# Optimization experiments

Hardware: AMD Instinct MI355X
Metric: run time of the kernel (lower is better)

Reference implementation:

```python
import jax, jax.numpy as jnp
import numpy as np

DIM = 1024
HEADS = 8
DIM_HEAD = 64
EPS = 1e-10
LN_EPS = 1e-5


def setup_inputs() -> dict:
    key = jax.random.key(0)
    k1, k2, k3 = jax.random.split(key, 3)
    b, n = 2, 4096
    x = jax.random.normal(k1, (b, n, DIM), dtype=jnp.float32)
    ln_gamma = jnp.ones((DIM,), dtype=jnp.float32)
    ln_beta = jnp.zeros((DIM,), dtype=jnp.float32)
    w_qkv = jax.random.normal(k2, (DIM, 3 * HEADS * DIM_HEAD), dtype=jnp.float32) * (DIM ** -0.5)
    w_out = jax.random.normal(k3, (HEADS * DIM_HEAD, DIM), dtype=jnp.float32) * ((HEADS * DIM_HEAD) ** -0.5)
    return {"x": x, "ln_gamma": ln_gamma, "ln_beta": ln_beta, "w_qkv": w_qkv, "w_out": w_out}


def _layernorm(x, gamma, beta):
    mu = jnp.mean(x, axis=-1, keepdims=True)
    var = jnp.var(x, axis=-1, keepdims=True)
    return (x - mu) * jax.lax.rsqrt(var + LN_EPS) * gamma + beta


def reference(x, ln_gamma, ln_beta, w_qkv, w_out):
    b, n, _ = x.shape
    h, dh = HEADS, DIM_HEAD
    scale = dh ** -0.5

    xn = _layernorm(x, ln_gamma, ln_beta)          # prenorm
    qkv = xn @ w_qkv                               # [b, n, 3*h*dh]
    q, k, v = jnp.split(qkv, 3, axis=-1)
    # [b, n, h*dh] -> [b, h, n, dh]
    def to_heads(t):
        return t.reshape(b, n, h, dh).transpose(0, 2, 1, 3)
    q, k, v = to_heads(q), to_heads(k), to_heads(v)

    # Ring/blockwise attention with online softmax is mathematically
    # equivalent to full softmax attention with an eps in the denominator.
    sim = jnp.einsum('bhid,bhjd->bhij', q, k) * scale   # [b, h, n, n]
    causal_mask = jnp.tril(jnp.ones((n, n), dtype=bool))
    sim = jnp.where(causal_mask, sim, -jnp.finfo(sim.dtype).max)

    m = jnp.max(sim, axis=-1, keepdims=True)            # row max (stable)
    p = jnp.exp(sim - m)
    denom = jnp.sum(p, axis=-1, keepdims=True) + EPS
    attn = p / denom

    out = jnp.einsum('bhij,bhjd->bhid', attn, v)        # [b, h, n, dh]
    out = out.transpose(0, 2, 1, 3).reshape(b, n, h * dh)
    return out @ w_out                                  # [b, n, dim]
```

## Files before the change

kernel.cpp:

```cpp
#include <hip/hip_runtime.h>
#include <hip/hip_bf16.h>
#include <stdint.h>

typedef unsigned short u16;
typedef unsigned int u32;

typedef __attribute__((ext_vector_type(8))) __bf16 bf16x8;
typedef __attribute__((ext_vector_type(4))) float f32x4;
typedef __attribute__((ext_vector_type(8))) u16 u16x8;

#define DIM 1024
#define SEQ 4096
#define NTOK 8192
#define NBH 16
#define NSLOT 136

static __device__ __forceinline__ float bf2f(u16 u) {
    union { u32 u; float f; } c; c.u = ((u32)u) << 16; return c.f;
}
static __device__ __forceinline__ u16 f2bf(float f) {
    union { float f; u32 u; } c; c.f = f;
    u32 u = c.u;
    return (u16)((u + 0x7FFF + ((u >> 16) & 1)) >> 16);
}
static __device__ __forceinline__ u16 cvt_bf16(float f) {
    union { __bf16 b; u16 u; } c; c.b = (__bf16)f;
    return c.u;
}
static __device__ __forceinline__ u32 pack_bf16(float lo, float hi) {
    return (u32)cvt_bf16(lo) | ((u32)cvt_bf16(hi) << 16);
}
static __device__ __forceinline__ f32x4 mfma_bf16(bf16x8 a, bf16x8 b, f32x4 c) {
    return __builtin_amdgcn_mfma_f32_16x16x32_bf16(a, b, c, 0, 0, 0);
}

typedef const __attribute__((address_space(1))) unsigned int* gptr_t;
typedef __attribute__((address_space(3))) unsigned int* lptr_t;

__global__ __launch_bounds__(256) void ln_kernel(const float* __restrict__ x,
                                                 const float* __restrict__ g,
                                                 const float* __restrict__ bta,
                                                 u16* __restrict__ xn) {
    int row = blockIdx.x;
    int tid = threadIdx.x;
    float4 v = ((const float4*)(x + (size_t)row * DIM))[tid];
    float f[4] = {v.x, v.y, v.z, v.w};
    float s = 0.f, s2 = 0.f;
#pragma unroll
    for (int i = 0; i < 4; i++) { s += f[i]; s2 += f[i] * f[i]; }
#pragma unroll
    for (int m = 1; m < 64; m <<= 1) { s += __shfl_xor(s, m); s2 += __shfl_xor(s2, m); }
    __shared__ float red[8];
    int w = tid >> 6;
    if ((tid & 63) == 0) { red[w * 2] = s; red[w * 2 + 1] = s2; }
    __syncthreads();
    s  = red[0] + red[2] + red[4] + red[6];
    s2 = red[1] + red[3] + red[5] + red[7];
    float mu = s * (1.f / DIM);
    float var = s2 * (1.f / DIM) - mu * mu;
    float rstd = rsqrtf(var + 1e-5f);
    u16 o[4];
#pragma unroll
    for (int i = 0; i < 4; i++) {
        int c = tid * 4 + i;
        o[i] = f2bf((f[i] - mu) * rstd * g[c] + bta[c]);
    }
    *(uint64_t*)(xn + (size_t)row * DIM + tid * 4) = *(uint64_t*)o;
}

__global__ __launch_bounds__(256) void transpose_kernel(const float* __restrict__ src,
                                                        u16* __restrict__ dst,
                                                        int R, int C) {
    __shared__ float t[32][33];
    int lx = threadIdx.x & 31, ly = threadIdx.x >> 5;
    int c = blockIdx.x * 32 + lx;
#pragma unroll
    for (int i = 0; i < 32; i += 8)
        t[ly + i][lx] = src[(size_t)(blockIdx.y * 32 + ly + i) * C + c];
    __syncthreads();
    int rr = blockIdx.y * 32 + lx;
#pragma unroll
    for (int i = 0; i < 32; i += 8)
        dst[(size_t)(blockIdx.x * 32 + ly + i) * R + rr] = f2bf(t[lx][ly + i]);
}

template <int K>
static __device__ __forceinline__ void gemm_core(const u16* __restrict__ A,
                                                 const u16* __restrict__ B,
                                                 int rowBase, int colBase,
                                                 u16* A_lds, u16* B_lds,
                                                 f32x4 acc[4][4]) {
    int tid = threadIdx.x;
    int lane = tid & 63;
    int l15 = lane & 15, q4 = lane >> 4;
    int w = tid >> 6;
    int wm = w >> 1, wn = w & 1;
#pragma unroll
    for (int mt = 0; mt < 4; mt++)
#pragma unroll
        for (int nt = 0; nt < 4; nt++) acc[mt][nt] = (f32x4){0.f, 0.f, 0.f, 0.f};

    char* Ab = (char*)A_lds;
    char* Bb = (char*)B_lds;

    for (int k0 = 0; k0 < K; k0 += 32) {
        __syncthreads();
#pragma unroll
        for (int i = 0; i < 2; i++) {
            int c = i * 256 + tid;
            int r = c >> 2;
            int piece = (c & 3) * 8;
            const u16* gA = A + (size_t)(rowBase + r) * K + k0 + piece;
            const u16* gB = B + (size_t)(colBase + r) * K + k0 + piece;
            unsigned ldsOff = (unsigned)(i * 4096 + w * 1024);
            __builtin_amdgcn_global_load_lds((gptr_t)gA, (lptr_t)(Ab + ldsOff), 16, 0, 0);
            __builtin_amdgcn_global_load_lds((gptr_t)gB, (lptr_t)(Bb + ldsOff), 16, 0, 0);
        }
        __syncthreads();
        bf16x8 a[4], b[4];
#pragma unroll
        for (int mt = 0; mt < 4; mt++)
            a[mt] = *(const bf16x8*)(A_lds + (wm * 64 + mt * 16 + l15) * 32 + q4 * 8);
#pragma unroll
        for (int nt = 0; nt < 4; nt++)
            b[nt] = *(const bf16x8*)(B_lds + (wn * 64 + nt * 16 + l15) * 32 + q4 * 8);
#pragma unroll
        for (int mt = 0; mt < 4; mt++)
#pragma unroll
            for (int nt = 0; nt < 4; nt++)
                acc[mt][nt] = mfma_bf16(a[mt], b[nt], acc[mt][nt]);
    }
}

__global__ __launch_bounds__(256) void gemm_qkv_kernel(const u16* __restrict__ xn,
                                                       const u16* __restrict__ wT,
                                                       u16* __restrict__ qb,
                                                       u16* __restrict__ kb,
                                                       u16* __restrict__ vbT) {
    __shared__ u16 A_lds[128 * 32];
    __shared__ u16 B_lds[128 * 32];
    f32x4 acc[4][4];
    gemm_core<1024>(xn, wT, blockIdx.x * 128, blockIdx.y * 128, A_lds, B_lds, acc);
    int lane = threadIdx.x & 63;
    int w = threadIdx.x >> 6;
    int wm = w >> 1, wn = w & 1;
    const float SC = 0.125f * 1.44269504f;
#pragma unroll
    for (int mt = 0; mt < 4; mt++) {
#pragma unroll
        for (int nt = 0; nt < 4; nt++) {
#pragma unroll
            for (int r = 0; r < 4; r++) {
                int m = blockIdx.x * 128 + wm * 64 + mt * 16 + (lane >> 4) * 4 + r;
                int n = blockIdx.y * 128 + wn * 64 + nt * 16 + (lane & 15);
                int piece = n >> 9;
                int c = n & 511;
                int h = c >> 6;
                int d = c & 63;
                int bi = m >> 12;
                int nn = m & 4095;
                int bh = bi * 8 + h;
                float av = acc[mt][nt][r];
                if (piece == 0)      qb[((size_t)(bh * SEQ + nn) << 6) + d] = f2bf(av * SC);
                else if (piece == 1) kb[((size_t)(bh * SEQ + nn) << 6) + d] = f2bf(av);
                else                 vbT[((size_t)(bh * 64 + d) << 12) + nn] = f2bf(av);
            }
        }
    }
}

__global__ __launch_bounds__(256) void gemm_out_kernel(const u16* __restrict__ aout,
                                                       const u16* __restrict__ wT,
                                                       float* __restrict__ out) {
    __shared__ u16 A_lds[128 * 32];
    __shared__ u16 B_lds[128 * 32];
    f32x4 acc[4][4];
    gemm_core<512>(aout, wT, blockIdx.x * 128, blockIdx.y * 128, A_lds, B_lds, acc);
    int lane = threadIdx.x & 63;
    int w = threadIdx.x >> 6;
    int wm = w >> 1, wn = w & 1;
#pragma unroll
    for (int mt = 0; mt < 4; mt++) {
#pragma unroll
        for (int nt = 0; nt < 4; nt++) {
#pragma unroll
            for (int r = 0; r < 4; r++) {
                int m = blockIdx.x * 128 + wm * 64 + mt * 16 + (lane >> 4) * 4 + r;
                int n = blockIdx.y * 128 + wn * 64 + nt * 16 + (lane & 15);
                out[(size_t)m * DIM + n] = acc[mt][nt][r];
            }
        }
    }
}


__global__ __launch_bounds__(256) void attn_partial_kernel(const u16* __restrict__ qb,
                                                           const u16* __restrict__ kb,
                                                           const u16* __restrict__ vbT,
                                                           u16* __restrict__ part,
                                                           float* __restrict__ lpart) {
    __shared__ u16 K_lds[4096];
    __shared__ u16 V_lds[4096];
    __shared__ u16 P_lds[4][1024];

    int bid = blockIdx.x;
    int bs = (bid & 7) * 272 + (bid >> 3);
    int idx = NBH * NSLOT - 1 - bs;
    int bh = idx / NSLOT;
    int s  = idx - bh * NSLOT;
    int qt, ci;
    if (s < 20)       { qt = s; ci = 0; }
    else if (s < 60)  { int t = s - 20;  qt = 20 + (t >> 1); ci = t & 1; }
    else if (s < 120) { int t = s - 60;  qt = 40 + t / 3;    ci = t - (t / 3) * 3; }
    else              { int t = s - 120; qt = 60 + (t >> 2); ci = t & 3; }
    int nq = qt + 1;
    int nc = (nq + 19) / 20;
    int L  = nq / nc;
    int R  = nq - L * nc;
    int kt0 = ci * L + (ci < R ? ci : R);
    int kt1 = kt0 + L + (ci < R ? 1 : 0) - 1;

    int tid = threadIdx.x;
    int lane = tid & 63;
    int l15 = lane & 15, g = lane >> 4;
    int w = tid >> 6;
    int swz = (l15 & 7) << 3;
    int rd0 = (g * 8) ^ swz;
    int rd1 = (32 + g * 8) ^ swz;

    const u16* Kp0 = kb + (size_t)bh * SEQ * 64;
    const u16* VTp = vbT + (size_t)bh * 64 * SEQ;

    const u16* qp = qb + ((size_t)bh * SEQ + (size_t)qt * 64 + w * 16 + l15) * 64;
    bf16x8 bQ0 = *(const bf16x8*)(qp + g * 8);
    bf16x8 bQ1 = *(const bf16x8*)(qp + 32 + g * 8);

    int c0 = tid, c1 = tid + 256;
    int r0 = c0 >> 3, g0 = c0 & 7;
    int r1 = c1 >> 3, g1 = c1 & 7;
    int wc0 = r0 * 64 + ((g0 ^ (r0 & 7)) * 8);
    int wc1 = r1 * 64 + ((g1 ^ (r1 & 7)) * 8);

    u16x8 krA0, krA1, vrA0, vrA1;
    {
        const u16* Kt = Kp0 + (size_t)kt0 * 4096;
        krA0 = *(const u16x8*)(Kt + r0 * 64 + g0 * 8);
        krA1 = *(const u16x8*)(Kt + r1 * 64 + g1 * 8);
        vrA0 = *(const u16x8*)(VTp + (size_t)r0 * SEQ + kt0 * 64 + g0 * 8);
        vrA1 = *(const u16x8*)(VTp + (size_t)r1 * SEQ + kt0 * 64 + g1 * 8);
    }

    f32x4 Oacc[4];
    f32x4 l_acc = (f32x4){0.f, 0.f, 0.f, 0.f};
#pragma unroll
    for (int vt = 0; vt < 4; vt++) Oacc[vt] = (f32x4){0.f, 0.f, 0.f, 0.f};

    const __bf16 one_bf = (__bf16)1.0f;
    bf16x8 vones = {one_bf, one_bf, one_bf, one_bf, one_bf, one_bf, one_bf, one_bf};

    u16* Pw = &P_lds[w][0];

    for (int kt = kt0; kt <= kt1; kt++) {
        __syncthreads();
        *(u16x8*)(K_lds + wc0) = krA0;
        *(u16x8*)(K_lds + wc1) = krA1;
        *(u16x8*)(V_lds + wc0) = vrA0;
        *(u16x8*)(V_lds + wc1) = vrA1;
        __syncthreads();
        int ktn = (kt < kt1) ? kt + 1 : kt1;
        {
            const u16* Ktn = Kp0 + (size_t)ktn * 4096;
            krA0 = *(const u16x8*)(Ktn + r0 * 64 + g0 * 8);
            krA1 = *(const u16x8*)(Ktn + r1 * 64 + g1 * 8);
            vrA0 = *(const u16x8*)(VTp + (size_t)r0 * SEQ + ktn * 64 + g0 * 8);
            vrA1 = *(const u16x8*)(VTp + (size_t)r1 * SEQ + ktn * 64 + g1 * 8);
        }

        f32x4 sv[4];
#pragma unroll
        for (int nt = 0; nt < 4; nt++) {
            int row = nt * 16 + l15;
            bf16x8 a0 = *(const bf16x8*)(K_lds + row * 64 + rd0);
            bf16x8 a1 = *(const bf16x8*)(K_lds + row * 64 + rd1);
            f32x4 z = (f32x4){0.f, 0.f, 0.f, 0.f};
            z = mfma_bf16(a0, bQ0, z);
            z = mfma_bf16(a1, bQ1, z);
            sv[nt] = z;
        }

        if (kt != qt) {
#pragma unroll
            for (int nt = 0; nt < 4; nt++) {
                uint2 t;
                t.x = pack_bf16(__builtin_amdgcn_exp2f(sv[nt][0]),
                                __builtin_amdgcn_exp2f(sv[nt][1]));
                t.y = pack_bf16(__builtin_amdgcn_exp2f(sv[nt][2]),
                                __builtin_amdgcn_exp2f(sv[nt][3]));
                *(uint2*)(Pw + l15 * 64 + ((nt * 16 + g * 4) ^ swz)) = t;
            }
        } else {
            int qg = w * 16 + l15;
#pragma unroll
            for (int nt = 0; nt < 4; nt++) {
                float p[4];
#pragma unroll
                for (int r = 0; r < 4; r++) {
                    int kg = nt * 16 + g * 4 + r;
                    p[r] = (kg <= qg) ? __builtin_amdgcn_exp2f(sv[nt][r]) : 0.f;
                }
                uint2 t;
                t.x = pack_bf16(p[0], p[1]);
                t.y = pack_bf16(p[2], p[3]);
                *(uint2*)(Pw + l15 * 64 + ((nt * 16 + g * 4) ^ swz)) = t;
            }
        }

        bf16x8 aP0 = *(const bf16x8*)(Pw + l15 * 64 + rd0);
        bf16x8 aP1 = *(const bf16x8*)(Pw + l15 * 64 + rd1);
        l_acc = mfma_bf16(aP0, vones, l_acc);
        l_acc = mfma_bf16(aP1, vones, l_acc);
#pragma unroll
        for (int vt = 0; vt < 4; vt++) {
            int vrow = vt * 16 + l15;
            bf16x8 bV0 = *(const bf16x8*)(V_lds + vrow * 64 + rd0);
            bf16x8 bV1 = *(const bf16x8*)(V_lds + vrow * 64 + rd1);
            Oacc[vt] = mfma_bf16(aP0, bV0, Oacc[vt]);
            Oacc[vt] = mfma_bf16(aP1, bV1, Oacc[vt]);
        }
    }

    u16* po = part + (size_t)idx * 4096;
#pragma unroll
    for (int vt = 0; vt < 4; vt++)
#pragma unroll
        for (int r = 0; r < 4; r++) {
            int q = w * 16 + g * 4 + r;
            int d = vt * 16 + l15;
            po[q * 64 + d] = f2bf(Oacc[vt][r]);
        }
    if (l15 == 0) {
#pragma unroll
        for (int r = 0; r < 4; r++)
            lpart[(size_t)idx * 64 + w * 16 + g * 4 + r] = l_acc[r];
    }
}

__global__ __launch_bounds__(256) void attn_combine_kernel(const u16* __restrict__ part,
                                                           const float* __restrict__ lpart,
                                                           u16* __restrict__ aout) {
    int bid = blockIdx.x;
    int bh = bid >> 6;
    int qt = bid & 63;
    int nc, base;
    if (qt < 20)      { nc = 1; base = qt; }
    else if (qt < 40) { nc = 2; base = 20 + (qt - 20) * 2; }
    else if (qt < 60) { nc = 3; base = 60 + (qt - 40) * 3; }
    else              { nc = 4; base = 120 + (qt - 60) * 4; }
    int sb = bh * NSLOT + base;

    int t = threadIdx.x;
    int q = t >> 2;
    int dg = (t & 3) * 16;

    float acc[16];
#pragma unroll
    for (int j = 0; j < 16; j++) acc[j] = 0.f;
    float ll = 0.f;
    for (int ci = 0; ci < nc; ci++) {
        const u16* pp = part + (size_t)(sb + ci) * 4096 + q * 64 + dg;
        u16x8 v0 = *(const u16x8*)pp;
        u16x8 v1 = *(const u16x8*)(pp + 8);
#pragma unroll
        for (int j = 0; j < 8; j++) { acc[j] += bf2f(v0[j]); acc[8 + j] += bf2f(v1[j]); }
        ll += lpart[(size_t)(sb + ci) * 64 + q];
    }
    float inv = 1.f / (ll + 1e-10f);
    int b = bh >> 3, h = bh & 7;
    size_t row = (size_t)(b * SEQ + qt * 64 + q);
    u16 o[16];
#pragma unroll
    for (int j = 0; j < 16; j++) o[j] = f2bf(acc[j] * inv);
    u16* dst = aout + row * 512 + h * 64 + dg;
    *(u16x8*)dst = *(u16x8*)o;
    *(u16x8*)(dst + 8) = *(u16x8*)(o + 8);
}

extern "C" void kernel_launch(void* const* d_in, const int* in_sizes, int n_in,
                              void* d_out, int out_size, void* d_ws, size_t ws_size,
                              hipStream_t stream) {
    const float* x    = (const float*)d_in[0];
    const float* g    = (const float*)d_in[1];
    const float* bta  = (const float*)d_in[2];
    const float* wqkv = (const float*)d_in[3];
    const float* wout = (const float*)d_in[4];
    float* out = (float*)d_out;

    char* ws = (char*)d_ws;
    size_t off = 0;
    auto alloc = [&](size_t bytes) {
        void* p = ws + off;
        off += (bytes + 255) & ~(size_t)255;
        return p;
    };
    u16* xn    = (u16*)alloc((size_t)NTOK * DIM * 2);
    u16* wqkvT = (u16*)alloc((size_t)1536 * 1024 * 2);
    u16* woutT = (u16*)alloc((size_t)1024 * 512 * 2);
    u16* qb    = (u16*)alloc((size_t)NBH * SEQ * 64 * 2);
    u16* kb    = (u16*)alloc((size_t)NBH * SEQ * 64 * 2);
    u16* vbT   = (u16*)alloc((size_t)NBH * SEQ * 64 * 2);
    u16* part  = xn;
    float* lpart = (float*)(xn + (size_t)NBH * NSLOT * 4096);
    u16* aout  = qb;

    ln_kernel<<<NTOK, 256, 0, stream>>>(x, g, bta, xn);
    transpose_kernel<<<dim3(1536 / 32, 1024 / 32), 256, 0, stream>>>(wqkv, wqkvT, 1024, 1536);
    transpose_kernel<<<dim3(1024 / 32, 512 / 32), 256, 0, stream>>>(wout, woutT, 512, 1024);
    gemm_qkv_kernel<<<dim3(64, 12), 256, 0, stream>>>(xn, wqkvT, qb, kb, vbT);
    attn_partial_kernel<<<NBH * NSLOT, 256, 0, stream>>>(qb, kb, vbT, part, lpart);
    attn_combine_kernel<<<NBH * 64, 256, 0, stream>>>(part, lpart, aout);
    gemm_out_kernel<<<dim3(64, 8), 256, 0, stream>>>(aout, woutT, out);
}
```

Baseline: 216.1 us.

## Halve attention block to two waves with two query subtiles each; merge prep kernels

The attention partial kernel now runs with 128 threads, and each wave handles 32 query rows as two 16-row subtiles. K fragments read from LDS are reused across both subtiles, and the V fragments are reused across both output accumulators, which cuts LDS reads per MFMA. Each thread loads twice as many K/V chunks per tile, and register pressure rises. LayerNorm and the two weight transposes are also merged into one launch to save launch overhead.

```diff
diff --git a/kernel.cpp b/kernel.cpp
--- a/kernel.cpp
+++ b/kernel.cpp
@@ -37,51 +37,60 @@
 typedef const __attribute__((address_space(1))) unsigned int* gptr_t;
 typedef __attribute__((address_space(3))) unsigned int* lptr_t;
 
-__global__ __launch_bounds__(256) void ln_kernel(const float* __restrict__ x,
-                                                 const float* __restrict__ g,
-                                                 const float* __restrict__ bta,
-                                                 u16* __restrict__ xn) {
-    int row = blockIdx.x;
+__global__ __launch_bounds__(256) void prep_kernel(const float* __restrict__ x,
+                                                   const float* __restrict__ g,
+                                                   const float* __restrict__ bta,
+                                                   u16* __restrict__ xn,
+                                                   const float* __restrict__ wqkv,
+                                                   u16* __restrict__ wqkvT,
+                                                   const float* __restrict__ wout,
+                                                   u16* __restrict__ woutT) {
+    __shared__ float red[8];
+    __shared__ float tT[32][33];
+    int bid = blockIdx.x;
     int tid = threadIdx.x;
-    float4 v = ((const float4*)(x + (size_t)row * DIM))[tid];
-    float f[4] = {v.x, v.y, v.z, v.w};
-    float s = 0.f, s2 = 0.f;
-#pragma unroll
-    for (int i = 0; i < 4; i++) { s += f[i]; s2 += f[i] * f[i]; }
-#pragma unroll
-    for (int m = 1; m < 64; m <<= 1) { s += __shfl_xor(s, m); s2 += __shfl_xor(s2, m); }
-    __shared__ float red[8];
-    int w = tid >> 6;
-    if ((tid & 63) == 0) { red[w * 2] = s; red[w * 2 + 1] = s2; }
+
+    if (bid < NTOK) {
+        int row = bid;
+        float4 v = ((const float4*)(x + (size_t)row * DIM))[tid];
+        float f[4] = {v.x, v.y, v.z, v.w};
+        float s = 0.f, s2 = 0.f;
+#pragma unroll
+        for (int i = 0; i < 4; i++) { s += f[i]; s2 += f[i] * f[i]; }
+#pragma unroll
+        for (int m = 1; m < 64; m <<= 1) { s += __shfl_xor(s, m); s2 += __shfl_xor(s2, m); }
+        int w = tid >> 6;
+        if ((tid & 63) == 0) { red[w * 2] = s; red[w * 2 + 1] = s2; }
+        __syncthreads();
+        s  = red[0] + red[2] + red[4] + red[6];
+        s2 = red[1] + red[3] + red[5] + red[7];
+        float mu = s * (1.f / DIM);
+        float var = s2 * (1.f / DIM) - mu * mu;
+        float rstd = rsqrtf(var + 1e-5f);
+        u16 o[4];
+#pragma unroll
+        for (int i = 0; i < 4; i++) {
+            int c = tid * 4 + i;
+            o[i] = f2bf((f[i] - mu) * rstd * g[c] + bta[c]);
+        }
+        *(uint64_t*)(xn + (size_t)row * DIM + tid * 4) = *(uint64_t*)o;
+        return;
+    }
+
+    int tt = bid - NTOK;
+    const float* src; u16* dst; int R, C, bx, by;
+    if (tt < 1536) { src = wqkv; dst = wqkvT; R = 1024; C = 1536; bx = tt % 48; by = tt / 48; }
+    else { tt -= 1536; src = wout; dst = woutT; R = 512; C = 1024; bx = tt & 31; by = tt >> 5; }
+    int lx = tid & 31, ly = tid >> 5;
+    int c = bx * 32 + lx;
+#pragma unroll
+    for (int i = 0; i < 32; i += 8)
+        tT[ly + i][lx] = src[(size_t)(by * 32 + ly + i) * C + c];
     __syncthreads();
-    s  = red[0] + red[2] + red[4] + red[6];
-    s2 = red[1] + red[3] + red[5] + red[7];
-    float mu = s * (1.f / DIM);
-    float var = s2 * (1.f / DIM) - mu * mu;
-    float rstd = rsqrtf(var + 1e-5f);
-    u16 o[4];
-#pragma unroll
-    for (int i = 0; i < 4; i++) {
-        int c = tid * 4 + i;
-        o[i] = f2bf((f[i] - mu) * rstd * g[c] + bta[c]);
-    }
-    *(uint64_t*)(xn + (size_t)row * DIM + tid * 4) = *(uint64_t*)o;
-}
-
-__global__ __launch_bounds__(256) void transpose_kernel(const float* __restrict__ src,
-                                                        u16* __restrict__ dst,
-                                                        int R, int C) {
-    __shared__ float t[32][33];
-    int lx = threadIdx.x & 31, ly = threadIdx.x >> 5;
-    int c = blockIdx.x * 32 + lx;
+    int rr = by * 32 + lx;
 #pragma unroll
     for (int i = 0; i < 32; i += 8)
-        t[ly + i][lx] = src[(size_t)(blockIdx.y * 32 + ly + i) * C + c];
-    __syncthreads();
-    int rr = blockIdx.y * 32 + lx;
-#pragma unroll
-    for (int i = 0; i < 32; i += 8)
-        dst[(size_t)(blockIdx.x * 32 + ly + i) * R + rr] = f2bf(t[lx][ly + i]);
+        dst[(size_t)(bx * 32 + ly + i) * R + rr] = f2bf(tT[lx][ly + i]);
 }
 
 template <int K>
@@ -194,14 +203,14 @@
 }
 
 
-__global__ __launch_bounds__(256) void attn_partial_kernel(const u16* __restrict__ qb,
+__global__ __launch_bounds__(128) void attn_partial_kernel(const u16* __restrict__ qb,
                                                            const u16* __restrict__ kb,
                                                            const u16* __restrict__ vbT,
                                                            u16* __restrict__ part,
                                                            float* __restrict__ lpart) {
     __shared__ u16 K_lds[4096];
     __shared__ u16 V_lds[4096];
-    __shared__ u16 P_lds[4][1024];
+    __shared__ u16 P_lds[2][1024];
 
     int bid = blockIdx.x;
     int bs = (bid & 7) * 272 + (bid >> 3);
@@ -231,29 +240,43 @@
     const u16* Kp0 = kb + (size_t)bh * SEQ * 64;
     const u16* VTp = vbT + (size_t)bh * 64 * SEQ;
 
-    const u16* qp = qb + ((size_t)bh * SEQ + (size_t)qt * 64 + w * 16 + l15) * 64;
-    bf16x8 bQ0 = *(const bf16x8*)(qp + g * 8);
-    bf16x8 bQ1 = *(const bf16x8*)(qp + 32 + g * 8);
-
-    int c0 = tid, c1 = tid + 256;
-    int r0 = c0 >> 3, g0 = c0 & 7;
-    int r1 = c1 >> 3, g1 = c1 & 7;
-    int wc0 = r0 * 64 + ((g0 ^ (r0 & 7)) * 8);
-    int wc1 = r1 * 64 + ((g1 ^ (r1 & 7)) * 8);
-
-    u16x8 krA0, krA1, vrA0, vrA1;
+    bf16x8 bQ[2][2];
+#pragma unroll
+    for (int qs = 0; qs < 2; qs++) {
+        const u16* qp = qb + ((size_t)bh * SEQ + (size_t)qt * 64 + w * 32 + qs * 16 + l15) * 64;
+        bQ[qs][0] = *(const bf16x8*)(qp + g * 8);
+        bQ[qs][1] = *(const bf16x8*)(qp + 32 + g * 8);
+    }
+
+    int wcc[4], soK[4];
+    size_t soV[4];
+#pragma unroll
+    for (int i = 0; i < 4; i++) {
+        int c = tid + 128 * i;
+        int r = c >> 3, gg = c & 7;
+        wcc[i] = r * 64 + ((gg ^ (r & 7)) * 8);
+        soK[i] = r * 64 + gg * 8;
+        soV[i] = (size_t)r * SEQ + gg * 8;
+    }
+
+    u16x8 krA[4], vrA[4];
     {
         const u16* Kt = Kp0 + (size_t)kt0 * 4096;
-        krA0 = *(const u16x8*)(Kt + r0 * 64 + g0 * 8);
-        krA1 = *(const u16x8*)(Kt + r1 * 64 + g1 * 8);
-        vrA0 = *(const u16x8*)(VTp + (size_t)r0 * SEQ + kt0 * 64 + g0 * 8);
-        vrA1 = *(const u16x8*)(VTp + (size_t)r1 * SEQ + kt0 * 64 + g1 * 8);
-    }
-
-    f32x4 Oacc[4];
-    f32x4 l_acc = (f32x4){0.f, 0.f, 0.f, 0.f};
-#pragma unroll
-    for (int vt = 0; vt < 4; vt++) Oacc[vt] = (f32x4){0.f, 0.f, 0.f, 0.f};
+#pragma unroll
+        for (int i = 0; i < 4; i++) {
+            krA[i] = *(const u16x8*)(Kt + soK[i]);
+            vrA[i] = *(const u16x8*)(VTp + soV[i] + kt0 * 64);
+        }
+    }
+
+    f32x4 Oacc[2][4];
+    f32x4 l_acc[2];
+#pragma unroll
+    for (int qs = 0; qs < 2; qs++) {
+        l_acc[qs] = (f32x4){0.f, 0.f, 0.f, 0.f};
+#pragma unroll
+        for (int vt = 0; vt < 4; vt++) Oacc[qs][vt] = (f32x4){0.f, 0.f, 0.f, 0.f};
+    }
 
     const __bf16 one_bf = (__bf16)1.0f;
     bf16x8 vones = {one_bf, one_bf, one_bf, one_bf, one_bf, one_bf, one_bf, one_bf};
@@ -262,86 +285,104 @@
 
     for (int kt = kt0; kt <= kt1; kt++) {
         __syncthreads();
-        *(u16x8*)(K_lds + wc0) = krA0;
-        *(u16x8*)(K_lds + wc1) = krA1;
-        *(u16x8*)(V_lds + wc0) = vrA0;
-        *(u16x8*)(V_lds + wc1) = vrA1;
+#pragma unroll
+        for (int i = 0; i < 4; i++) {
+            *(u16x8*)(K_lds + wcc[i]) = krA[i];
+            *(u16x8*)(V_lds + wcc[i]) = vrA[i];
+        }
         __syncthreads();
         int ktn = (kt < kt1) ? kt + 1 : kt1;
         {
             const u16* Ktn = Kp0 + (size_t)ktn * 4096;
-            krA0 = *(const u16x8*)(Ktn + r0 * 64 + g0 * 8);
-            krA1 = *(const u16x8*)(Ktn + r1 * 64 + g1 * 8);
-            vrA0 = *(const u16x8*)(VTp + (size_t)r0 * SEQ + ktn * 64 + g0 * 8);
-            vrA1 = *(const u16x8*)(VTp + (size_t)r1 * SEQ + ktn * 64 + g1 * 8);
-        }
-
-        f32x4 sv[4];
+#pragma unroll
+            for (int i = 0; i < 4; i++) {
+                krA[i] = *(const u16x8*)(Ktn + soK[i]);
+                vrA[i] = *(const u16x8*)(VTp + soV[i] + ktn * 64);
+            }
+        }
+
+        bf16x8 ka[4][2];
 #pragma unroll
         for (int nt = 0; nt < 4; nt++) {
             int row = nt * 16 + l15;
-            bf16x8 a0 = *(const bf16x8*)(K_lds + row * 64 + rd0);
-            bf16x8 a1 = *(const bf16x8*)(K_lds + row * 64 + rd1);
-            f32x4 z = (f32x4){0.f, 0.f, 0.f, 0.f};
-            z = mfma_bf16(a0, bQ0, z);
-            z = mfma_bf16(a1, bQ1, z);
-            sv[nt] = z;
-        }
-
-        if (kt != qt) {
+            ka[nt][0] = *(const bf16x8*)(K_lds + row * 64 + rd0);
+            ka[nt][1] = *(const bf16x8*)(K_lds + row * 64 + rd1);
+        }
+
+        bf16x8 aP[2][2];
+#pragma unroll
+        for (int qs = 0; qs < 2; qs++) {
+            f32x4 sv[4];
 #pragma unroll
             for (int nt = 0; nt < 4; nt++) {
-                uint2 t;
-                t.x = pack_bf16(__builtin_amdgcn_exp2f(sv[nt][0]),
-                                __builtin_amdgcn_exp2f(sv[nt][1]));
-                t.y = pack_bf16(__builtin_amdgcn_exp2f(sv[nt][2]),
-                                __builtin_amdgcn_exp2f(sv[nt][3]));
-                *(uint2*)(Pw + l15 * 64 + ((nt * 16 + g * 4) ^ swz)) = t;
-            }
-        } else {
-            int qg = w * 16 + l15;
-#pragma unroll
-            for (int nt = 0; nt < 4; nt++) {
-                float p[4];
-#pragma unroll
-                for (int r = 0; r < 4; r++) {
-                    int kg = nt * 16 + g * 4 + r;
-                    p[r] = (kg <= qg) ? __builtin_amdgcn_exp2f(sv[nt][r]) : 0.f;
+                f32x4 z = (f32x4){0.f, 0.f, 0.f, 0.f};
+                z = mfma_bf16(ka[nt][0], bQ[qs][0], z);
+                z = mfma_bf16(ka[nt][1], bQ[qs][1], z);
+                sv[nt] = z;
+            }
+
+            if (kt != qt) {
+#pragma unroll
+                for (int nt = 0; nt < 4; nt++) {
+                    uint2 t;
+                    t.x = pack_bf16(__builtin_amdgcn_exp2f(sv[nt][0]),
+                                    __builtin_amdgcn_exp2f(sv[nt][1]));
+                    t.y = pack_bf16(__builtin_amdgcn_exp2f(sv[nt][2]),
+                                    __builtin_amdgcn_exp2f(sv[nt][3]));
+                    *(uint2*)(Pw + l15 * 64 + ((nt * 16 + g * 4) ^ swz)) = t;
                 }
-                uint2 t;
-                t.x = pack_bf16(p[0], p[1]);
-                t.y = pack_bf16(p[2], p[3]);
-                *(uint2*)(Pw + l15 * 64 + ((nt * 16 + g * 4) ^ swz)) = t;
-            }
-        }
-
-        bf16x8 aP0 = *(const bf16x8*)(Pw + l15 * 64 + rd0);
-        bf16x8 aP1 = *(const bf16x8*)(Pw + l15 * 64 + rd1);
-        l_acc = mfma_bf16(aP0, vones, l_acc);
-        l_acc = mfma_bf16(aP1, vones, l_acc);
+            } else {
+                int qg = w * 32 + qs * 16 + l15;
+#pragma unroll
+                for (int nt = 0; nt < 4; nt++) {
+                    float p[4];
+#pragma unroll
+                    for (int r = 0; r < 4; r++) {
+                        int kg = nt * 16 + g * 4 + r;
+                        p[r] = (kg <= qg) ? __builtin_amdgcn_exp2f(sv[nt][r]) : 0.f;
+                    }
+                    uint2 t;
+                    t.x = pack_bf16(p[0], p[1]);
+                    t.y = pack_bf16(p[2], p[3]);
+                    *(uint2*)(Pw + l15 * 64 + ((nt * 16 + g * 4) ^ swz)) = t;
+                }
+            }
+
+            aP[qs][0] = *(const bf16x8*)(Pw + l15 * 64 + rd0);
+            aP[qs][1] = *(const bf16x8*)(Pw + l15 * 64 + rd1);
+            l_acc[qs] = mfma_bf16(aP[qs][0], vones, l_acc[qs]);
+            l_acc[qs] = mfma_bf16(aP[qs][1], vones, l_acc[qs]);
+        }
+
 #pragma unroll
         for (int vt = 0; vt < 4; vt++) {
             int vrow = vt * 16 + l15;
             bf16x8 bV0 = *(const bf16x8*)(V_lds + vrow * 64 + rd0);
             bf16x8 bV1 = *(const bf16x8*)(V_lds + vrow * 64 + rd1);
-            Oacc[vt] = mfma_bf16(aP0, bV0, Oacc[vt]);
-            Oacc[vt] = mfma_bf16(aP1, bV1, Oacc[vt]);
+#pragma unroll
+            for (int qs = 0; qs < 2; qs++) {
+                Oacc[qs][vt] = mfma_bf16(aP[qs][0], bV0, Oacc[qs][vt]);
+                Oacc[qs][vt] = mfma_bf16(aP[qs][1], bV1, Oacc[qs][vt]);
+            }
         }
     }
 
     u16* po = part + (size_t)idx * 4096;
 #pragma unroll
-    for (int vt = 0; vt < 4; vt++)
-#pragma unroll
-        for (int r = 0; r < 4; r++) {
-            int q = w * 16 + g * 4 + r;
-            int d = vt * 16 + l15;
-            po[q * 64 + d] = f2bf(Oacc[vt][r]);
-        }
-    if (l15 == 0) {
-#pragma unroll
-        for (int r = 0; r < 4; r++)
-            lpart[(size_t)idx * 64 + w * 16 + g * 4 + r] = l_acc[r];
+    for (int qs = 0; qs < 2; qs++) {
+#pragma unroll
+        for (int vt = 0; vt < 4; vt++)
+#pragma unroll
+            for (int r = 0; r < 4; r++) {
+                int q = w * 32 + qs * 16 + g * 4 + r;
+                int d = vt * 16 + l15;
+                po[q * 64 + d] = f2bf(Oacc[qs][vt][r]);
+            }
+        if (l15 == 0) {
+#pragma unroll
+            for (int r = 0; r < 4; r++)
+                lpart[(size_t)idx * 64 + w * 32 + qs * 16 + g * 4 + r] = l_acc[qs][r];
+        }
     }
 }
 
@@ -412,11 +453,9 @@
     float* lpart = (float*)(xn + (size_t)NBH * NSLOT * 4096);
     u16* aout  = qb;
 
-    ln_kernel<<<NTOK, 256, 0, stream>>>(x, g, bta, xn);
-    transpose_kernel<<<dim3(1536 / 32, 1024 / 32), 256, 0, stream>>>(wqkv, wqkvT, 1024, 1536);
-    transpose_kernel<<<dim3(1024 / 32, 512 / 32), 256, 0, stream>>>(wout, woutT, 512, 1024);
+    prep_kernel<<<NTOK + 1536 + 512, 256, 0, stream>>>(x, g, bta, xn, wqkv, wqkvT, wout, woutT);
     gemm_qkv_kernel<<<dim3(64, 12), 256, 0, stream>>>(xn, wqkvT, qb, kb, vbT);
-    attn_partial_kernel<<<NBH * NSLOT, 256, 0, stream>>>(qb, kb, vbT, part, lpart);
+    attn_partial_kernel<<<NBH * NSLOT, 128, 0, stream>>>(qb, kb, vbT, part, lpart);
     attn_combine_kernel<<<NBH * 64, 256, 0, stream>>>(part, lpart, aout);
     gemm_out_kernel<<<dim3(64, 8), 256, 0, stream>>>(aout, woutT, out);
 }
```

Measured after the change: 210.4 us. 2.7% less time.
